# Optimization experiments

Measured on AMD Instinct MI355X. Metric: run time of the kernel, lower is better.

Reference implementation:

```python
import jax, jax.numpy as jnp
import numpy as np

B, N, DIM, H = 8, 1024, 1024, 16
D = DIM // H  # head dim = 64
SCALE = DIM ** (-0.5)  # NOTE: original uses full dim, not head dim


def setup_inputs() -> dict:
    key = jax.random.key(0)
    ks = jax.random.split(key, 8)
    x = jax.random.normal(ks[0], (B, N, DIM), dtype=jnp.float32)
    pos = jax.random.normal(ks[1], (B, N, DIM), dtype=jnp.float32)
    mask = jax.random.bernoulli(ks[2], 0.9, (B, N - 1))  # bool, [b, n-1]
    w_std = 0.02
    W_qk = jax.random.normal(ks[3], (2 * DIM, DIM), dtype=jnp.float32) * w_std  # Linear(dim, 2*dim_qk)
    W_v = jax.random.normal(ks[4], (DIM, DIM), dtype=jnp.float32) * w_std
    W_out = jax.random.normal(ks[5], (DIM, DIM), dtype=jnp.float32) * w_std
    b_out = jax.random.normal(ks[6], (DIM,), dtype=jnp.float32) * w_std
    return {"x": x, "mask": mask, "pos": pos, "W_qk": W_qk, "W_v": W_v,
            "W_out": W_out, "b_out": b_out}


def _split_heads(t):
    # b n (h d) -> b h n d
    b, n, _ = t.shape
    return t.reshape(b, n, H, D).transpose(0, 2, 1, 3)


def reference(x, mask, pos, W_qk, W_v, W_out, b_out):
    qk = x @ W_qk.T                       # [b, n, 2*dim]
    q, k = jnp.split(qk, 2, axis=-1)
    v = x @ W_v.T                         # [b, n, dim]
    q, k, v = _split_heads(q), _split_heads(k), _split_heads(v)  # [b,h,n,d]
    hpos = _split_heads(pos)
    q = q + hpos
    k = k + hpos
    dots = jnp.einsum('bhid,bhjd->bhij', q, k) * SCALE  # [b,h,n,n]
    mask_value = -jnp.finfo(dots.dtype).max
    # pad mask with True at position 0 (CLS token always visible)
    m = jnp.pad(mask, ((0, 0), (1, 0)), constant_values=True)  # [b, n]
    m2 = m[:, None, :] & m[:, :, None]                          # [b, n, n]
    dots = jnp.where(m2[:, None, :, :], dots, mask_value)
    attn = jax.nn.softmax(dots, axis=-1)
    out = jnp.einsum('bhij,bhjd->bhid', attn, v)  # [b,h,n,d]
    out = out.transpose(0, 2, 1, 3).reshape(x.shape[0], x.shape[1], DIM)  # b n (h d)
    out = out @ W_out.T + b_out  # dropout p=0.0 -> identity
    return out
```

## Files before the change

kernel.cpp:

```cpp
#include <hip/hip_runtime.h>


typedef unsigned short u16;
typedef short bf16x8 __attribute__((ext_vector_type(8)));
typedef float f32x4 __attribute__((ext_vector_type(4)));
typedef float f32x16 __attribute__((ext_vector_type(16)));

#define MFMA16(a, b, c) __builtin_amdgcn_mfma_f32_16x16x32_bf16((a), (b), (c), 0, 0, 0)
#define MFMA32(a, b, c) __builtin_amdgcn_mfma_f32_32x32x16_bf16((a), (b), (c), 0, 0, 0)

__device__ __forceinline__ u16 f2bf(float f) {
    union { float f; unsigned u; } x; x.f = f;
    unsigned r = x.u + 0x7fffu + ((x.u >> 16) & 1u);
    return (u16)(r >> 16);
}

__device__ __forceinline__ void gld16(const u16* g, u16* l) {
    __builtin_amdgcn_global_load_lds(
        (const __attribute__((address_space(1))) void*)g,
        (__attribute__((address_space(3))) void*)l, 16, 0, 0);
}

__global__ __launch_bounds__(256) void cast_all(
    const float* __restrict__ x, const float* __restrict__ wqk,
    const float* __restrict__ wv, const float* __restrict__ wout,
    u16* __restrict__ xbf, u16* __restrict__ wqkvbf, u16* __restrict__ woutbf) {
    int i = blockIdx.x * 256 + threadIdx.x;
    const float* src; u16* dst; int off;
    if (i < 2097152)      { src = x;    dst = xbf;              off = i; }
    else if (i < 2621440) { src = wqk;  dst = wqkvbf;           off = i - 2097152; }
    else if (i < 2883584) { src = wv;   dst = wqkvbf + 2097152; off = i - 2621440; }
    else                  { src = wout; dst = woutbf;           off = i - 2883584; }
    float4 v = ((const float4*)src)[off];
    ushort4 o;
    o.x = f2bf(v.x); o.y = f2bf(v.y); o.z = f2bf(v.z); o.w = f2bf(v.w);
    ((ushort4*)dst)[off] = o;
}

__global__ __launch_bounds__(256) void gemm_qk(
    const u16* __restrict__ A,
    const u16* __restrict__ Bw,
    const float* __restrict__ pos,
    u16* __restrict__ Q, u16* __restrict__ Kx) {
    const int n0 = blockIdx.x * 128, m0 = blockIdx.y * 128;
    const int t = threadIdx.x, w = t >> 6, ln = t & 63;
    const int l15 = ln & 15, l4 = ln >> 4;
    const int wm = (w >> 1) * 64, wn = (w & 1) * 64;

    __shared__ u16 As[128 * 64];
    __shared__ u16 Bs[128 * 64];

    f32x4 acc[4][4];
#pragma unroll
    for (int i = 0; i < 4; ++i)
#pragma unroll
        for (int j = 0; j < 4; ++j) acc[i][j] = (f32x4){0.f, 0.f, 0.f, 0.f};

    const int sr = ln >> 3;
    const int scx = ((ln & 7) ^ sr) * 8;
    const int x0 = (l15 & 7);
    for (int k0 = 0; k0 < 1024; k0 += 64) {
        __syncthreads();
#pragma unroll
        for (int p = 0; p < 4; ++p) {
            int rbase = w * 32 + p * 8;
            gld16(A  + (size_t)(m0 + rbase + sr) * 1024 + k0 + scx, &As[rbase * 64]);
            gld16(Bw + (size_t)(n0 + rbase + sr) * 1024 + k0 + scx, &Bs[rbase * 64]);
        }
        __syncthreads();
#pragma unroll
        for (int kt = 0; kt < 2; ++kt) {
            bf16x8 a[4], bfr[4];
#pragma unroll
            for (int mt = 0; mt < 4; ++mt)
                a[mt] = *(const bf16x8*)&As[(wm + mt * 16 + l15) * 64 + ((kt * 4 + l4) ^ x0) * 8];
#pragma unroll
            for (int nt = 0; nt < 4; ++nt)
                bfr[nt] = *(const bf16x8*)&Bs[(wn + nt * 16 + l15) * 64 + ((kt * 4 + l4) ^ x0) * 8];
#pragma unroll
            for (int mt = 0; mt < 4; ++mt)
#pragma unroll
                for (int nt = 0; nt < 4; ++nt)
                    acc[mt][nt] = MFMA16(a[mt], bfr[nt], acc[mt][nt]);
        }
    }
#pragma unroll
    for (int mt = 0; mt < 4; ++mt)
#pragma unroll
        for (int nt = 0; nt < 4; ++nt)
#pragma unroll
            for (int r = 0; r < 4; ++r) {
                int i = m0 + wm + mt * 16 + l4 * 4 + r;
                int j = n0 + wn + nt * 16 + l15;
                int bb = i >> 10, n = i & 1023;
                int jj = j & 1023;
                float v = acc[mt][nt][r] + pos[(size_t)i * 1024 + jj];
                int hh = jj >> 6, dd = jj & 63;
                size_t idx = (((size_t)(bb * 16 + hh)) * 1024 + n) * 64 + dd;
                if (j < 1024) Q[idx] = f2bf(v * 0.045084220027780106f);
                else          Kx[idx] = f2bf(v);
            }
}

__global__ __launch_bounds__(256) void zero_k(
    const int* __restrict__ maskIn,
    u16* __restrict__ Kx) {
    int tid = blockIdx.x * 256 + threadIdx.x;
    int seg = tid & 7;
    int row = tid >> 3;
    int n = row & 1023;
    int b = row >> 14;
    if (n == 0) return;
    if (maskIn[b * 1023 + n - 1] != 0) return;
    uint4 z = {0u, 0u, 0u, 0u};
    *(uint4*)(Kx + (size_t)row * 64 + seg * 8) = z;
}

__global__ __launch_bounds__(256) void gemm_v(
    const u16* __restrict__ Wv,
    const u16* __restrict__ X,
    u16* __restrict__ Vt) {
    const int n0 = blockIdx.x * 128, m0 = blockIdx.y * 128;
    const int bIdx = blockIdx.z;
    const u16* Xb = X + (size_t)bIdx * 1048576;
    const int t = threadIdx.x, w = t >> 6, ln = t & 63;
    const int l15 = ln & 15, l4 = ln >> 4;
    const int wm = (w >> 1) * 64, wn = (w & 1) * 64;

    __shared__ u16 As[128 * 64];
    __shared__ u16 Bs[128 * 64];

    f32x4 acc[4][4];
#pragma unroll
    for (int i = 0; i < 4; ++i)
#pragma unroll
        for (int j = 0; j < 4; ++j) acc[i][j] = (f32x4){0.f, 0.f, 0.f, 0.f};

    const int sr = ln >> 3;
    const int scx = ((ln & 7) ^ sr) * 8;
    const int x0 = (l15 & 7);
    for (int k0 = 0; k0 < 1024; k0 += 64) {
        __syncthreads();
#pragma unroll
        for (int p = 0; p < 4; ++p) {
            int rbase = w * 32 + p * 8;
            gld16(Wv + (size_t)(m0 + rbase + sr) * 1024 + k0 + scx, &As[rbase * 64]);
            gld16(Xb + (size_t)(n0 + rbase + sr) * 1024 + k0 + scx, &Bs[rbase * 64]);
        }
        __syncthreads();
#pragma unroll
        for (int kt = 0; kt < 2; ++kt) {
            bf16x8 a[4], bfr[4];
#pragma unroll
            for (int mt = 0; mt < 4; ++mt)
                a[mt] = *(const bf16x8*)&As[(wm + mt * 16 + l15) * 64 + ((kt * 4 + l4) ^ x0) * 8];
#pragma unroll
            for (int nt = 0; nt < 4; ++nt)
                bfr[nt] = *(const bf16x8*)&Bs[(wn + nt * 16 + l15) * 64 + ((kt * 4 + l4) ^ x0) * 8];
#pragma unroll
            for (int mt = 0; mt < 4; ++mt)
#pragma unroll
                for (int nt = 0; nt < 4; ++nt)
                    acc[mt][nt] = MFMA16(a[mt], bfr[nt], acc[mt][nt]);
        }
    }
#pragma unroll
    for (int mt = 0; mt < 4; ++mt)
#pragma unroll
        for (int nt = 0; nt < 4; ++nt)
#pragma unroll
            for (int r = 0; r < 4; ++r) {
                int i = m0 + wm + mt * 16 + l4 * 4 + r;
                int j = n0 + wn + nt * 16 + l15;
                Vt[((size_t)(bIdx * 1024 + i)) * 1024 + j] = f2bf(acc[mt][nt][r]);
            }
}

__global__ __launch_bounds__(64) void vsum_kernel(const u16* __restrict__ Vt,
                                                  const int* __restrict__ maskIn,
                                                  float* __restrict__ Vsum,
                                                  float* __restrict__ Vmask) {
    int row = blockIdx.x, ln = threadIdx.x;
    int b = row >> 10;
    const u16* p = Vt + (size_t)row * 1024 + ln * 16;
    uint4 a = *(const uint4*)p;
    uint4 bq = *(const uint4*)(p + 8);
    float s = 0.f, sm = 0.f;
    unsigned vv[8] = {a.x, a.y, a.z, a.w, bq.x, bq.y, bq.z, bq.w};
#pragma unroll
    for (int i = 0; i < 8; ++i) {
        int j0 = ln * 16 + 2 * i;
        float lo = __uint_as_float(vv[i] << 16);
        float hi = __uint_as_float(vv[i] & 0xffff0000u);
        s += lo + hi;
        bool ok0 = (j0 == 0) || (maskIn[b * 1023 + j0 - 1] != 0);
        bool ok1 = (maskIn[b * 1023 + j0] != 0);
        if (!ok0) sm += lo;
        if (!ok1) sm += hi;
    }
#pragma unroll
    for (int d = 1; d < 64; d <<= 1) { s += __shfl_xor(s, d); sm += __shfl_xor(sm, d); }
    if (ln == 0) { Vsum[row] = s; Vmask[row] = sm; }
}

__global__ __launch_bounds__(512) void attn_kernel(
    const u16* __restrict__ Q,
    const u16* __restrict__ Kx,
    const u16* __restrict__ Vt,
    const int* __restrict__ maskIn,
    const float* __restrict__ Vsum,
    const float* __restrict__ Vmask,
    u16* __restrict__ O) {
    const int gid = blockIdx.x;
    const int bh = gid & 127;
    const int qt = gid >> 7;
    const int b = bh >> 4, h = bh & 15;
    const int t = threadIdx.x, w = t >> 6, ln = t & 63;
    const int half = w >> 2, wq = w & 3;
    const int l31 = ln & 31, l5 = ln >> 5;

    __shared__ __align__(16) char lds[65568];
    float* nm = (float*)(lds + 65536);

    {
        float cnt = 0.f;
        for (int i = t; i < 1023; i += 512)
            cnt += (maskIn[b * 1023 + i] == 0) ? 1.f : 0.f;
#pragma unroll
        for (int d = 1; d < 64; d <<= 1) cnt += __shfl_xor(cnt, d);
        if (ln == 0) nm[w] = cnt;
    }

    const size_t qkbase = (size_t)bh * 65536;
    const int q0 = qt * 128 + wq * 32;
    const int q = q0 + l31;

    bf16x8 bq[4];
#pragma unroll
    for (int kt = 0; kt < 4; ++kt)
        bq[kt] = *(const bf16x8*)(Q + qkbase + (size_t)q * 64 + kt * 16 + l5 * 8);

    float lsum = 0.f;
    f32x16 o0 = {0,0,0,0,0,0,0,0,0,0,0,0,0,0,0,0};
    f32x16 o1 = {0,0,0,0,0,0,0,0,0,0,0,0,0,0,0,0};

    const int jbase = half * 512;
    const int srow = ln >> 3;
    const int swz8 = (ln & 7) ^ srow;
    u16* ldsH = (u16*)(lds + half * 32768);
    const int rb = wq * 16;

#define ATTN_STAGE(c, j0_)                                                              \
    do {                                                                                \
        gld16(Kx + qkbase + (size_t)((j0_) + rb + srow) * 64 + swz8 * 8,                \
              ldsH + (c) * 8192 + rb * 64);                                             \
        gld16(Kx + qkbase + (size_t)((j0_) + rb + 8 + srow) * 64 + swz8 * 8,            \
              ldsH + (c) * 8192 + (rb + 8) * 64);                                       \
        gld16(Vt + qkbase + (size_t)(rb + srow) * 1024 + (j0_) + swz8 * 8,              \
              ldsH + (c) * 8192 + 4096 + rb * 64);                                      \
        gld16(Vt + qkbase + (size_t)(rb + 8 + srow) * 1024 + (j0_) + swz8 * 8,          \
              ldsH + (c) * 8192 + 4096 + (rb + 8) * 64);                                \
    } while (0)

    ATTN_STAGE(0, jbase);
    int cur = 0;
    for (int jt = 0; jt < 8; ++jt) {
        const int j0 = jbase + jt * 64;
        if (jt < 7) {
            ATTN_STAGE(cur ^ 1, j0 + 64);
            asm volatile("s_waitcnt vmcnt(4)" ::: "memory");
        } else {
            asm volatile("s_waitcnt vmcnt(0)" ::: "memory");
        }
        __builtin_amdgcn_s_barrier();

        const u16* Kb = ldsH + cur * 8192;
        const u16* Vb = Kb + 4096;

        f32x16 st0 = {0,0,0,0,0,0,0,0,0,0,0,0,0,0,0,0};
        f32x16 st1 = {0,0,0,0,0,0,0,0,0,0,0,0,0,0,0,0};
        __builtin_amdgcn_s_setprio(1);
#pragma unroll
        for (int ktk = 0; ktk < 4; ++ktk) {
            const int sw = ((ktk * 2 + l5) ^ (l31 & 7)) * 8;
            bf16x8 ak0 = *(const bf16x8*)&Kb[l31 * 64 + sw];
            bf16x8 ak1 = *(const bf16x8*)&Kb[(32 + l31) * 64 + sw];
            st0 = MFMA32(ak0, bq[ktk], st0);
            st1 = MFMA32(ak1, bq[ktk], st1);
        }
        __builtin_amdgcn_s_setprio(0);
#pragma unroll
        for (int i = 0; i < 16; ++i) {
            float p0 = __builtin_amdgcn_exp2f(st0[i]);
            float p1 = __builtin_amdgcn_exp2f(st1[i]);
            st0[i] = p0;
            st1[i] = p1;
            lsum += p0 + p1;
        }
        unsigned pk0[8], pk1[8];
#pragma unroll
        for (int g = 0; g < 4; ++g) {
#pragma unroll
            for (int qq = 0; qq < 2; ++qq) {
                unsigned a0 = __float_as_uint(st0[g * 4 + 2 * qq]) + 0x8000u;
                unsigned a1 = __float_as_uint(st0[g * 4 + 2 * qq + 1]) + 0x8000u;
                pk0[2 * g + qq] = (a1 & 0xffff0000u) | (a0 >> 16);
                unsigned c0 = __float_as_uint(st1[g * 4 + 2 * qq]) + 0x8000u;
                unsigned c1 = __float_as_uint(st1[g * 4 + 2 * qq + 1]) + 0x8000u;
                pk1[2 * g + qq] = (c1 & 0xffff0000u) | (c0 >> 16);
            }
        }
        bf16x8 pf[4];
#pragma unroll
        for (int kt = 0; kt < 4; ++kt) {
            const int hh = kt & 1;
            unsigned own0, own1, off0, off1;
            if (kt < 2) {
                own0 = l5 ? pk0[4 * hh + 2] : pk0[4 * hh];
                own1 = l5 ? pk0[4 * hh + 3] : pk0[4 * hh + 1];
                off0 = l5 ? pk0[4 * hh]     : pk0[4 * hh + 2];
                off1 = l5 ? pk0[4 * hh + 1] : pk0[4 * hh + 3];
            } else {
                own0 = l5 ? pk1[4 * hh + 2] : pk1[4 * hh];
                own1 = l5 ? pk1[4 * hh + 3] : pk1[4 * hh + 1];
                off0 = l5 ? pk1[4 * hh]     : pk1[4 * hh + 2];
                off1 = l5 ? pk1[4 * hh + 1] : pk1[4 * hh + 3];
            }
            unsigned ex0 = (unsigned)__shfl_xor((int)off0, 32);
            unsigned ex1 = (unsigned)__shfl_xor((int)off1, 32);
            unsigned dw0 = l5 ? ex0 : own0;
            unsigned dw1 = l5 ? ex1 : own1;
            unsigned dw2 = l5 ? own0 : ex0;
            unsigned dw3 = l5 ? own1 : ex1;
            union { unsigned u[4]; bf16x8 v; } cv;
            cv.u[0] = dw0; cv.u[1] = dw1; cv.u[2] = dw2; cv.u[3] = dw3;
            pf[kt] = cv.v;
        }
        __builtin_amdgcn_s_setprio(1);
#pragma unroll
        for (int kt = 0; kt < 4; ++kt) {
            const int sw = ((kt * 2 + l5) ^ (l31 & 7)) * 8;
            bf16x8 av0 = *(const bf16x8*)&Vb[l31 * 64 + sw];
            bf16x8 av1 = *(const bf16x8*)&Vb[(32 + l31) * 64 + sw];
            o0 = MFMA32(av0, pf[kt], o0);
            o1 = MFMA32(av1, pf[kt], o1);
        }
        __builtin_amdgcn_s_setprio(0);
        __builtin_amdgcn_sched_barrier(0);
        __builtin_amdgcn_s_barrier();
        cur ^= 1;
    }
#undef ATTN_STAGE

    float* comb = (float*)lds;
    if (half == 1) {
        float* dst = comb + ((size_t)(wq * 64 + ln)) * 33;
#pragma unroll
        for (int i = 0; i < 16; ++i) { dst[i] = o0[i]; dst[16 + i] = o1[i]; }
        dst[32] = lsum;
    }
    __syncthreads();
    if (half == 0) {
        const float* src = comb + ((size_t)(wq * 64 + ln)) * 33;
#pragma unroll
        for (int i = 0; i < 16; ++i) { o0[i] += src[i]; o1[i] += src[16 + i]; }
        lsum += src[32];
        float lrow = lsum + __shfl_xor(lsum, 32);
        float nmaskb = nm[0] + nm[1] + nm[2] + nm[3] + nm[4] + nm[5] + nm[6] + nm[7];
        lrow -= nmaskb;
        const float linv = 1.f / lrow;
        const int n = q0 + l31;
        const bool rqv = (n == 0) || (maskIn[b * 1023 + n - 1] != 0);
        u16* orow = O + ((size_t)(b * 1024 + n)) * 1024 + h * 64;
#pragma unroll
        for (int g = 0; g < 4; ++g) {
            ushort4 s0, s1;
            unsigned short* p0 = (unsigned short*)&s0;
            unsigned short* p1 = (unsigned short*)&s1;
#pragma unroll
            for (int r = 0; r < 4; ++r) {
                int reg = 4 * g + r;
                int d0 = 8 * g + 4 * l5 + r;
                float v0 = rqv ? (o0[reg] - Vmask[bh * 64 + d0]) * linv
                               : Vsum[bh * 64 + d0] * 0.0009765625f;
                float v1 = rqv ? (o1[reg] - Vmask[bh * 64 + 32 + d0]) * linv
                               : Vsum[bh * 64 + 32 + d0] * 0.0009765625f;
                p0[r] = f2bf(v0);
                p1[r] = f2bf(v1);
            }
            *(ushort4*)&orow[8 * g + 4 * l5] = s0;
            *(ushort4*)&orow[32 + 8 * g + 4 * l5] = s1;
        }
    }
}

__global__ __launch_bounds__(256) void gemm_out(
    const u16* __restrict__ A,
    const u16* __restrict__ Bw,
    const float* __restrict__ bias,
    float* __restrict__ out) {
    const int n0 = blockIdx.x * 128, m0 = blockIdx.y * 128;
    const int t = threadIdx.x, w = t >> 6, ln = t & 63;
    const int l15 = ln & 15, l4 = ln >> 4;
    const int wm = (w >> 1) * 64, wn = (w & 1) * 64;

    __shared__ u16 As[128 * 64];
    __shared__ u16 Bs[128 * 64];

    f32x4 acc[4][4];
#pragma unroll
    for (int i = 0; i < 4; ++i)
#pragma unroll
        for (int j = 0; j < 4; ++j) acc[i][j] = (f32x4){0.f, 0.f, 0.f, 0.f};

    const int sr = ln >> 3;
    const int scx = ((ln & 7) ^ sr) * 8;
    const int x0 = (l15 & 7);
    for (int k0 = 0; k0 < 1024; k0 += 64) {
        __syncthreads();
#pragma unroll
        for (int p = 0; p < 4; ++p) {
            int rbase = w * 32 + p * 8;
            gld16(A  + (size_t)(m0 + rbase + sr) * 1024 + k0 + scx, &As[rbase * 64]);
            gld16(Bw + (size_t)(n0 + rbase + sr) * 1024 + k0 + scx, &Bs[rbase * 64]);
        }
        __syncthreads();
#pragma unroll
        for (int kt = 0; kt < 2; ++kt) {
            bf16x8 a[4], bfr[4];
#pragma unroll
            for (int mt = 0; mt < 4; ++mt)
                a[mt] = *(const bf16x8*)&As[(wm + mt * 16 + l15) * 64 + ((kt * 4 + l4) ^ x0) * 8];
#pragma unroll
            for (int nt = 0; nt < 4; ++nt)
                bfr[nt] = *(const bf16x8*)&Bs[(wn + nt * 16 + l15) * 64 + ((kt * 4 + l4) ^ x0) * 8];
#pragma unroll
            for (int mt = 0; mt < 4; ++mt)
#pragma unroll
                for (int nt = 0; nt < 4; ++nt)
                    acc[mt][nt] = MFMA16(a[mt], bfr[nt], acc[mt][nt]);
        }
    }
#pragma unroll
    for (int mt = 0; mt < 4; ++mt)
#pragma unroll
        for (int nt = 0; nt < 4; ++nt)
#pragma unroll
            for (int r = 0; r < 4; ++r) {
                int i = m0 + wm + mt * 16 + l4 * 4 + r;
                int j = n0 + wn + nt * 16 + l15;
                out[(size_t)i * 1024 + j] = acc[mt][nt][r] + bias[j];
            }
}

extern "C" void kernel_launch(void* const* d_in, const int* in_sizes, int n_in,
                              void* d_out, int out_size, void* d_ws, size_t ws_size,
                              hipStream_t stream) {
    const float* x    = (const float*)d_in[0];
    const int*   mask = (const int*)d_in[1];
    const float* pos  = (const float*)d_in[2];
    const float* wqk  = (const float*)d_in[3];
    const float* wv   = (const float*)d_in[4];
    const float* wout = (const float*)d_in[5];
    const float* bout = (const float*)d_in[6];

    char* ws = (char*)d_ws;
    u16* xbf    = (u16*)(ws + 0);
    u16* wqkvbf = (u16*)(ws + 16777216);
    u16* woutbf = (u16*)(ws + 23068672);
    u16* Qb     = (u16*)(ws + 25165824);
    u16* Kb     = (u16*)(ws + 41943040);
    u16* Vtb    = (u16*)(ws + 58720256);
    float* Vsum = (float*)(ws + 16777216);
    float* Vmask = (float*)(ws + 16777216 + 32768);

    cast_all<<<12288, 256, 0, stream>>>(x, wqk, wv, wout, xbf, wqkvbf, woutbf);

    gemm_qk<<<dim3(16, 64), 256, 0, stream>>>(xbf, wqkvbf, pos, Qb, Kb);
    zero_k<<<4096, 256, 0, stream>>>(mask, Kb);
    gemm_v<<<dim3(8, 8, 8), 256, 0, stream>>>(wqkvbf + 2097152, xbf, Vtb);
    vsum_kernel<<<8192, 64, 0, stream>>>(Vtb, mask, Vsum, Vmask);
    attn_kernel<<<1024, 512, 0, stream>>>(Qb, Kb, Vtb, mask, Vsum, Vmask, xbf);
    gemm_out<<<dim3(8, 64), 256, 0, stream>>>(xbf, woutbf, bout, (float*)d_out);
}
```

Baseline: 294.6 us.

## Double-buffer LDS tiles in the three projection GEMMs to overlap loads with MFMA

The qk, v and output-projection GEMMs now hold two LDS stages and issue the global-to-LDS loads for the next k-tile before computing on the current one. Partial vmcnt waits and raw s_barrier replace the two __syncthreads per iteration. The aim is to hide global load latency behind MFMA work. In exchange LDS use per block doubles to 64KB, which may lower occupancy, and correctness depends on the hand-written vmcnt counts matching the 8 loads issued per stage.

```diff
diff --git a/kernel.cpp b/kernel.cpp
--- a/kernel.cpp
+++ b/kernel.cpp
@@ -37,6 +37,18 @@
     ((ushort4*)dst)[off] = o;
 }
 
+#define GEMM_STAGE(c, k0_, PA, PB)                                                     \
+    do {                                                                               \
+        _Pragma("unroll")                                                              \
+        for (int p = 0; p < 4; ++p) {                                                  \
+            int rbase = w * 32 + p * 8;                                                \
+            gld16((PA) + (size_t)(m0 + rbase + sr) * 1024 + (k0_) + scx,               \
+                  &SS[c][0][rbase * 64]);                                              \
+            gld16((PB) + (size_t)(n0 + rbase + sr) * 1024 + (k0_) + scx,               \
+                  &SS[c][1][rbase * 64]);                                              \
+        }                                                                              \
+    } while (0)
+
 __global__ __launch_bounds__(256) void gemm_qk(
     const u16* __restrict__ A,
     const u16* __restrict__ Bw,
@@ -47,8 +59,7 @@
     const int l15 = ln & 15, l4 = ln >> 4;
     const int wm = (w >> 1) * 64, wn = (w & 1) * 64;
 
-    __shared__ u16 As[128 * 64];
-    __shared__ u16 Bs[128 * 64];
+    __shared__ u16 SS[2][2][128 * 64];
 
     f32x4 acc[4][4];
 #pragma unroll
@@ -59,30 +70,37 @@
     const int sr = ln >> 3;
     const int scx = ((ln & 7) ^ sr) * 8;
     const int x0 = (l15 & 7);
+
+    GEMM_STAGE(0, 0, A, Bw);
+    int cur = 0;
     for (int k0 = 0; k0 < 1024; k0 += 64) {
-        __syncthreads();
-#pragma unroll
-        for (int p = 0; p < 4; ++p) {
-            int rbase = w * 32 + p * 8;
-            gld16(A  + (size_t)(m0 + rbase + sr) * 1024 + k0 + scx, &As[rbase * 64]);
-            gld16(Bw + (size_t)(n0 + rbase + sr) * 1024 + k0 + scx, &Bs[rbase * 64]);
-        }
-        __syncthreads();
+        if (k0 < 960) {
+            GEMM_STAGE(cur ^ 1, k0 + 64, A, Bw);
+            asm volatile("s_waitcnt vmcnt(8)" ::: "memory");
+        } else {
+            asm volatile("s_waitcnt vmcnt(0)" ::: "memory");
+        }
+        __builtin_amdgcn_s_barrier();
+        const u16* Asb = SS[cur][0];
+        const u16* Bsb = SS[cur][1];
 #pragma unroll
         for (int kt = 0; kt < 2; ++kt) {
             bf16x8 a[4], bfr[4];
 #pragma unroll
             for (int mt = 0; mt < 4; ++mt)
-                a[mt] = *(const bf16x8*)&As[(wm + mt * 16 + l15) * 64 + ((kt * 4 + l4) ^ x0) * 8];
+                a[mt] = *(const bf16x8*)&Asb[(wm + mt * 16 + l15) * 64 + ((kt * 4 + l4) ^ x0) * 8];
 #pragma unroll
             for (int nt = 0; nt < 4; ++nt)
-                bfr[nt] = *(const bf16x8*)&Bs[(wn + nt * 16 + l15) * 64 + ((kt * 4 + l4) ^ x0) * 8];
+                bfr[nt] = *(const bf16x8*)&Bsb[(wn + nt * 16 + l15) * 64 + ((kt * 4 + l4) ^ x0) * 8];
 #pragma unroll
             for (int mt = 0; mt < 4; ++mt)
 #pragma unroll
                 for (int nt = 0; nt < 4; ++nt)
                     acc[mt][nt] = MFMA16(a[mt], bfr[nt], acc[mt][nt]);
         }
+        __builtin_amdgcn_sched_barrier(0);
+        __builtin_amdgcn_s_barrier();
+        cur ^= 1;
     }
 #pragma unroll
     for (int mt = 0; mt < 4; ++mt)
@@ -127,8 +145,7 @@
     const int l15 = ln & 15, l4 = ln >> 4;
     const int wm = (w >> 1) * 64, wn = (w & 1) * 64;
 
-    __shared__ u16 As[128 * 64];
-    __shared__ u16 Bs[128 * 64];
+    __shared__ u16 SS[2][2][128 * 64];
 
     f32x4 acc[4][4];
 #pragma unroll
@@ -139,30 +156,37 @@
     const int sr = ln >> 3;
     const int scx = ((ln & 7) ^ sr) * 8;
     const int x0 = (l15 & 7);
+
+    GEMM_STAGE(0, 0, Wv, Xb);
+    int cur = 0;
     for (int k0 = 0; k0 < 1024; k0 += 64) {
-        __syncthreads();
-#pragma unroll
-        for (int p = 0; p < 4; ++p) {
-            int rbase = w * 32 + p * 8;
-            gld16(Wv + (size_t)(m0 + rbase + sr) * 1024 + k0 + scx, &As[rbase * 64]);
-            gld16(Xb + (size_t)(n0 + rbase + sr) * 1024 + k0 + scx, &Bs[rbase * 64]);
-        }
-        __syncthreads();
+        if (k0 < 960) {
+            GEMM_STAGE(cur ^ 1, k0 + 64, Wv, Xb);
+            asm volatile("s_waitcnt vmcnt(8)" ::: "memory");
+        } else {
+            asm volatile("s_waitcnt vmcnt(0)" ::: "memory");
+        }
+        __builtin_amdgcn_s_barrier();
+        const u16* Asb = SS[cur][0];
+        const u16* Bsb = SS[cur][1];
 #pragma unroll
         for (int kt = 0; kt < 2; ++kt) {
             bf16x8 a[4], bfr[4];
 #pragma unroll
             for (int mt = 0; mt < 4; ++mt)
-                a[mt] = *(const bf16x8*)&As[(wm + mt * 16 + l15) * 64 + ((kt * 4 + l4) ^ x0) * 8];
+                a[mt] = *(const bf16x8*)&Asb[(wm + mt * 16 + l15) * 64 + ((kt * 4 + l4) ^ x0) * 8];
 #pragma unroll
             for (int nt = 0; nt < 4; ++nt)
-                bfr[nt] = *(const bf16x8*)&Bs[(wn + nt * 16 + l15) * 64 + ((kt * 4 + l4) ^ x0) * 8];
+                bfr[nt] = *(const bf16x8*)&Bsb[(wn + nt * 16 + l15) * 64 + ((kt * 4 + l4) ^ x0) * 8];
 #pragma unroll
             for (int mt = 0; mt < 4; ++mt)
 #pragma unroll
                 for (int nt = 0; nt < 4; ++nt)
                     acc[mt][nt] = MFMA16(a[mt], bfr[nt], acc[mt][nt]);
         }
+        __builtin_amdgcn_sched_barrier(0);
+        __builtin_amdgcn_s_barrier();
+        cur ^= 1;
     }
 #pragma unroll
     for (int mt = 0; mt < 4; ++mt)
@@ -404,8 +428,7 @@
     const int l15 = ln & 15, l4 = ln >> 4;
     const int wm = (w >> 1) * 64, wn = (w & 1) * 64;
 
-    __shared__ u16 As[128 * 64];
-    __shared__ u16 Bs[128 * 64];
+    __shared__ u16 SS[2][2][128 * 64];
 
     f32x4 acc[4][4];
 #pragma unroll
@@ -416,30 +439,37 @@
     const int sr = ln >> 3;
     const int scx = ((ln & 7) ^ sr) * 8;
     const int x0 = (l15 & 7);
+
+    GEMM_STAGE(0, 0, A, Bw);
+    int cur = 0;
     for (int k0 = 0; k0 < 1024; k0 += 64) {
-        __syncthreads();
-#pragma unroll
-        for (int p = 0; p < 4; ++p) {
-            int rbase = w * 32 + p * 8;
-            gld16(A  + (size_t)(m0 + rbase + sr) * 1024 + k0 + scx, &As[rbase * 64]);
-            gld16(Bw + (size_t)(n0 + rbase + sr) * 1024 + k0 + scx, &Bs[rbase * 64]);
-        }
-        __syncthreads();
+        if (k0 < 960) {
+            GEMM_STAGE(cur ^ 1, k0 + 64, A, Bw);
+            asm volatile("s_waitcnt vmcnt(8)" ::: "memory");
+        } else {
+            asm volatile("s_waitcnt vmcnt(0)" ::: "memory");
+        }
+        __builtin_amdgcn_s_barrier();
+        const u16* Asb = SS[cur][0];
+        const u16* Bsb = SS[cur][1];
 #pragma unroll
         for (int kt = 0; kt < 2; ++kt) {
             bf16x8 a[4], bfr[4];
 #pragma unroll
             for (int mt = 0; mt < 4; ++mt)
-                a[mt] = *(const bf16x8*)&As[(wm + mt * 16 + l15) * 64 + ((kt * 4 + l4) ^ x0) * 8];
+                a[mt] = *(const bf16x8*)&Asb[(wm + mt * 16 + l15) * 64 + ((kt * 4 + l4) ^ x0) * 8];
 #pragma unroll
             for (int nt = 0; nt < 4; ++nt)
-                bfr[nt] = *(const bf16x8*)&Bs[(wn + nt * 16 + l15) * 64 + ((kt * 4 + l4) ^ x0) * 8];
+                bfr[nt] = *(const bf16x8*)&Bsb[(wn + nt * 16 + l15) * 64 + ((kt * 4 + l4) ^ x0) * 8];
 #pragma unroll
             for (int mt = 0; mt < 4; ++mt)
 #pragma unroll
                 for (int nt = 0; nt < 4; ++nt)
                     acc[mt][nt] = MFMA16(a[mt], bfr[nt], acc[mt][nt]);
         }
+        __builtin_amdgcn_sched_barrier(0);
+        __builtin_amdgcn_s_barrier();
+        cur ^= 1;
     }
 #pragma unroll
     for (int mt = 0; mt < 4; ++mt)
```

Result: no change. 290.6 us (-1.4%).
